# Performance work log

Measured on AMD Instinct MI355X. Metric: run time of the kernel, lower is better.

The kernel has to match this reference:

```python
import jax, jax.numpy as jnp
import numpy as np

H = 12          # num heads
D = 768         # embed dim
HD = D // H     # head dim
SCALE = HD ** -0.5
NEG = -(3.0 ** 39)  # matches torch's triu(1) * -3.0**39 mask value


def setup_inputs() -> dict:
    key = jax.random.key(0)
    ks = jax.random.split(key, 9)
    B, S = 4, 1024
    lim = 1.0 / np.sqrt(D)
    def lin(k):
        kw, kb = jax.random.split(k)
        W = jax.random.uniform(kw, (D, D), jnp.float32, -lim, lim)  # [out,in]
        b = jax.random.uniform(kb, (D,), jnp.float32, -lim, lim)
        return W, b
    Wq, bq = lin(ks[0]); Wk, bk = lin(ks[1]); Wv, bv = lin(ks[2]); Wo, bo = lin(ks[3])
    hidden_states = jax.random.normal(ks[4], (B, S, D), jnp.float32)
    return {"hidden_states": hidden_states,
            "Wq": Wq, "bq": bq, "Wk": Wk, "bk": bk,
            "Wv": Wv, "bv": bv, "Wo": Wo, "bo": bo}


def reference(hidden_states, Wq, bq, Wk, bk, Wv, bv, Wo, bo):
    B, S, _ = hidden_states.shape
    split = lambda x: x.reshape(B, S, H, HD).transpose(0, 2, 1, 3)  # [B,H,S,HD]
    q = split(hidden_states @ Wq.T + bq) * SCALE
    k = split(hidden_states @ Wk.T + bk)
    v = split(hidden_states @ Wv.T + bv)
    scores = jnp.einsum('bhqd,bhkd->bhqk', q, k)
    causal_mask = jnp.triu(jnp.full((S, S), NEG, hidden_states.dtype), k=1)
    scores = scores + causal_mask  # broadcast over [B,H]
    probs = jax.nn.softmax(scores, axis=-1)
    out = jnp.einsum('bhqk,bhkd->bhqd', probs, v)
    out = out.transpose(0, 2, 1, 3).reshape(B, S, H * HD)
    return out @ Wo.T + bo
```

## Files before the change

kernel.cpp:

```cpp
#include <hip/hip_runtime.h>

#define NH 12
#define DM 768
#define HD 64
#define BB 4
#define SS 1024
#define MTOT (BB*SS)
#define ATT_SCALE 0.125f
#define NEGMASK (-4.0525551530189755e18f)

typedef __attribute__((ext_vector_type(8))) short short8;
typedef __attribute__((ext_vector_type(4))) float floatx4;
typedef __attribute__((ext_vector_type(4))) unsigned short ushort4v;

__device__ __forceinline__ float bf2f(unsigned short u){
    union { unsigned int i; float f; } x; x.i = ((unsigned int)u) << 16; return x.f;
}
__device__ __forceinline__ unsigned short f2bf(float f){
    union { float f; unsigned int i; } x; x.f = f;
    unsigned int i = x.i;
    return (unsigned short)((i + 0x7FFFu + ((i >> 16) & 1u)) >> 16);
}

#define XQ4 (MTOT*DM/4)
#define WQ4 (DM*DM/4)

__global__ __launch_bounds__(256) void convert_bf16(
    const float* __restrict__ X,
    const float* __restrict__ Wq, const float* __restrict__ Wk,
    const float* __restrict__ Wv, const float* __restrict__ Wo,
    unsigned short* __restrict__ Xb,
    unsigned short* __restrict__ Wqb, unsigned short* __restrict__ Wkb,
    unsigned short* __restrict__ Wvb, unsigned short* __restrict__ Wob)
{
    const int idx = blockIdx.x * 256 + threadIdx.x;
    const float* s; unsigned short* d; int off;
    if (idx < XQ4) { s = X; d = Xb; off = idx; }
    else {
        const int r = idx - XQ4;
        const int wsel = r / WQ4;
        off = r - wsel * WQ4;
        s = (wsel==0)?Wq:(wsel==1)?Wk:(wsel==2)?Wv:Wo;
        d = (wsel==0)?Wqb:(wsel==1)?Wkb:(wsel==2)?Wvb:Wob;
    }
    const float4 v = ((const float4*)s)[off];
    ushort4v o;
    o[0] = f2bf(v.x); o[1] = f2bf(v.y); o[2] = f2bf(v.z); o[3] = f2bf(v.w);
    ((ushort4v*)d)[off] = o;
}

__global__ __launch_bounds__(256) void qkv_mfma(
    const unsigned short* __restrict__ Xb,
    const unsigned short* __restrict__ Wqb,
    const unsigned short* __restrict__ Wkb,
    const unsigned short* __restrict__ Wvb,
    const float* __restrict__ bq, const float* __restrict__ bk,
    const float* __restrict__ bv,
    unsigned short* __restrict__ qout,
    unsigned short* __restrict__ kout,
    unsigned short* __restrict__ vout)
{
    const int which = blockIdx.z;
    const int n0 = blockIdx.x * 64;
    const int m0 = blockIdx.y * 128;
    const unsigned short* W = (which==0) ? Wqb : (which==1) ? Wkb : Wvb;
    const float* bias = (which==0) ? bq : (which==1) ? bk : bv;
    const float scl = (which==0) ? ATT_SCALE : 1.0f;

    __shared__ unsigned short As[128*32];
    __shared__ unsigned short Bs[64*32];

    const int t = threadIdx.x;
    const int w = t >> 6, lane = t & 63;
    const int c = lane & 15, g = lane >> 4;
    const int wr = w >> 1, wc = w & 1;

    floatx4 acc[4][2] = {};

    const int srow = lane >> 2;
    const int ske  = (lane & 3) * 8;

    for (int k0 = 0; k0 < DM; k0 += 32) {
        __syncthreads();
        #pragma unroll
        for (int j = 0; j < 2; ++j) {
            const int row = w*32 + j*16 + srow;
            __builtin_amdgcn_global_load_lds(
                (const __attribute__((address_space(1))) unsigned int*)
                    (Xb + (size_t)(m0 + row) * DM + k0 + ske),
                (__attribute__((address_space(3))) unsigned int*)
                    (As + (w*32 + j*16) * 32),
                16, 0, 0);
        }
        {
            const int row = w*16 + srow;
            __builtin_amdgcn_global_load_lds(
                (const __attribute__((address_space(1))) unsigned int*)
                    (W + (size_t)(n0 + row) * DM + k0 + ske),
                (__attribute__((address_space(3))) unsigned int*)
                    (Bs + (w*16) * 32),
                16, 0, 0);
        }
        __syncthreads();

        short8 af[4], bfr[2];
        #pragma unroll
        for (int mi = 0; mi < 4; ++mi)
            af[mi] = *(const short8*)(As + (wr*64 + mi*16 + c)*32 + g*8);
        #pragma unroll
        for (int ni = 0; ni < 2; ++ni)
            bfr[ni] = *(const short8*)(Bs + (wc*32 + ni*16 + c)*32 + g*8);
        #pragma unroll
        for (int mi = 0; mi < 4; ++mi)
            #pragma unroll
            for (int ni = 0; ni < 2; ++ni)
                acc[mi][ni] = __builtin_amdgcn_mfma_f32_16x16x32_bf16(
                    af[mi], bfr[ni], acc[mi][ni], 0, 0, 0);
    }

    #pragma unroll
    for (int mi = 0; mi < 4; ++mi) {
        #pragma unroll
        for (int r = 0; r < 4; ++r) {
            const int m = m0 + wr*64 + mi*16 + g*4 + r;
            const int b = m >> 10, s = m & 1023;
            #pragma unroll
            for (int ni = 0; ni < 2; ++ni) {
                const int n = n0 + wc*32 + ni*16 + c;
                const int h = n >> 6, hd = n & 63;
                const float val = (acc[mi][ni][r] + bias[n]) * scl;
                if (which == 2)
                    vout[(((size_t)(b*NH + h))*HD + hd)*SS + s] = f2bf(val);
                else if (which == 1)
                    kout[(((size_t)(b*NH + h))*SS + s)*HD + hd] = f2bf(val);
                else
                    qout[(((size_t)(b*NH + h))*SS + s)*HD + hd] = f2bf(val);
            }
        }
    }
}

__device__ __forceinline__ void stage_tile(
    const unsigned short* __restrict__ Kp,
    const unsigned short* __restrict__ VTp,
    int k0, int w, int lane,
    unsigned short* __restrict__ Ks,
    unsigned short* __restrict__ Vs)
{
    const int rsub = lane >> 3;
    const int cc   = (lane & 7) ^ rsub;
    #pragma unroll
    for (int j = 0; j < 2; ++j) {
        const int r = w*16 + j*8 + rsub;
        __builtin_amdgcn_global_load_lds(
            (const __attribute__((address_space(1))) unsigned int*)
                (Kp + (size_t)(k0 + r) * HD + cc*8),
            (__attribute__((address_space(3))) unsigned int*)
                (Ks + (w*16 + j*8) * HD),
            16, 0, 0);
        __builtin_amdgcn_global_load_lds(
            (const __attribute__((address_space(1))) unsigned int*)
                (VTp + (size_t)r * SS + k0 + cc*8),
            (__attribute__((address_space(3))) unsigned int*)
                (Vs + (w*16 + j*8) * HD),
            16, 0, 0);
    }
}

__device__ __forceinline__ void attn_process_tile(
    const unsigned short* __restrict__ Ks,
    const unsigned short* __restrict__ Vs,
    const short8 (&qf)[2],
    int k0, bool islast, int qg, int c, int g,
    float& m_c, float& l_c, floatx4 (&Oacc)[4],
    unsigned short* __restrict__ Pl)
{
    floatx4 S[4] = {};
    #pragma unroll
    for (int nf = 0; nf < 4; ++nf) {
        const int row = nf*16 + c;
        #pragma unroll
        for (int st = 0; st < 2; ++st) {
            const short8 kf = *(const short8*)(Ks + row*HD + (((g + 4*st) ^ (c & 7)) * 8));
            S[nf] = __builtin_amdgcn_mfma_f32_16x16x32_bf16(kf, qf[st], S[nf], 0, 0, 0);
        }
    }

    if (islast) {
        #pragma unroll
        for (int nf = 0; nf < 4; ++nf) {
            #pragma unroll
            for (int r = 0; r < 4; ++r) {
                const int key = k0 + nf*16 + g*4 + r;
                if (key > qg) S[nf][r] += NEGMASK;
            }
        }
    }

    float mx = -INFINITY;
    #pragma unroll
    for (int nf = 0; nf < 4; ++nf)
        #pragma unroll
        for (int r = 0; r < 4; ++r) mx = fmaxf(mx, S[nf][r]);
    mx = fmaxf(mx, __shfl_xor(mx, 16, 64));
    mx = fmaxf(mx, __shfl_xor(mx, 32, 64));
    const float mnew = fmaxf(m_c, mx);
    const float alpha = __expf(m_c - mnew);
    float sum = 0.0f;
    #pragma unroll
    for (int nf = 0; nf < 4; ++nf)
        #pragma unroll
        for (int r = 0; r < 4; ++r) {
            const float p = __expf(S[nf][r] - mnew);
            S[nf][r] = p;
            sum += p;
        }
    sum += __shfl_xor(sum, 16, 64);
    sum += __shfl_xor(sum, 32, 64);
    l_c = l_c * alpha + sum;
    m_c = mnew;
    #pragma unroll
    for (int nf = 0; nf < 4; ++nf)
        #pragma unroll
        for (int r = 0; r < 4; ++r) Oacc[nf][r] *= alpha;

    #pragma unroll
    for (int nf = 0; nf < 4; ++nf)
        #pragma unroll
        for (int r = 0; r < 4; ++r)
            Pl[c * 72 + nf*16 + g*4 + r] = f2bf(S[nf][r]);

    #pragma unroll
    for (int st = 0; st < 2; ++st) {
        const short8 pf = *(const short8*)(Pl + c * 72 + g*8 + 32*st);
        #pragma unroll
        for (int nf = 0; nf < 4; ++nf) {
            const int row = nf*16 + c;
            const short8 vf = *(const short8*)(Vs + row*HD + (((g + 4*st) ^ (c & 7)) * 8));
            Oacc[nf] = __builtin_amdgcn_mfma_f32_16x16x32_bf16(vf, pf, Oacc[nf], 0, 0, 0);
        }
    }
}

__global__ __launch_bounds__(256) void attn_mfma(
    const unsigned short* __restrict__ Q,
    const unsigned short* __restrict__ K,
    const unsigned short* __restrict__ VT,
    unsigned short* __restrict__ O)
{
    const int idx = blockIdx.x;
    const int bh  = idx % 48;
    const int z   = 15 - (idx / 48);
    const int q0  = z * 64;

    const unsigned short* Qp  = Q  + (size_t)bh * SS * HD;
    const unsigned short* Kp  = K  + (size_t)bh * SS * HD;
    const unsigned short* VTp = VT + (size_t)bh * HD * SS;

    __shared__ unsigned short Ks[2][64*HD];
    __shared__ unsigned short Vs[2][64*HD];
    __shared__ unsigned short Pl[4][16*72];

    const int t    = threadIdx.x;
    const int w    = t >> 6;
    const int lane = t & 63;
    const int c    = lane & 15;
    const int g    = lane >> 4;
    const int qg   = q0 + w*16 + c;

    short8 qf[2];
    #pragma unroll
    for (int st = 0; st < 2; ++st)
        qf[st] = *(const short8*)(Qp + (size_t)qg * HD + g*8 + 32*st);

    floatx4 Oacc[4] = {};
    float m_c = -INFINITY, l_c = 0.0f;

    const int ntile = z + 1;

    stage_tile(Kp, VTp, 0, w, lane, Ks[0], Vs[0]);
    __syncthreads();

    for (int kt = 0; kt < ntile; ++kt) {
        const int cur = kt & 1;
        if (kt + 1 < ntile)
            stage_tile(Kp, VTp, (kt+1)*64, w, lane, Ks[cur^1], Vs[cur^1]);
        attn_process_tile(Ks[cur], Vs[cur], qf, kt*64, kt == ntile-1,
                          qg, c, g, m_c, l_c, Oacc, Pl[w]);
        if (kt + 1 < ntile)
            __syncthreads();
    }

    const int b = bh / NH, h = bh % NH;
    const float inv = 1.0f / l_c;
    unsigned short* op = O + ((size_t)(b*SS + qg))*DM + h*HD;
    #pragma unroll
    for (int nf = 0; nf < 4; ++nf) {
        ushort4v o4;
        #pragma unroll
        for (int r = 0; r < 4; ++r) o4[r] = f2bf(Oacc[nf][r] * inv);
        *(ushort4v*)(op + nf*16 + g*4) = o4;
    }
}

__global__ __launch_bounds__(256) void out_mfma(
    const unsigned short* __restrict__ A,
    const unsigned short* __restrict__ Wb,
    const float* __restrict__ bias,
    float* __restrict__ outf)
{
    const int n0 = blockIdx.x * 64;
    const int m0 = blockIdx.y * 128;

    __shared__ unsigned short As[128*32];
    __shared__ unsigned short Bs[64*32];

    const int t = threadIdx.x;
    const int w = t >> 6, lane = t & 63;
    const int c = lane & 15, g = lane >> 4;
    const int wr = w >> 1, wc = w & 1;

    floatx4 acc[4][2] = {};

    const int srow = lane >> 2;
    const int ske  = (lane & 3) * 8;

    for (int k0 = 0; k0 < DM; k0 += 32) {
        __syncthreads();
        #pragma unroll
        for (int j = 0; j < 2; ++j) {
            const int row = w*32 + j*16 + srow;
            __builtin_amdgcn_global_load_lds(
                (const __attribute__((address_space(1))) unsigned int*)
                    (A + (size_t)(m0 + row) * DM + k0 + ske),
                (__attribute__((address_space(3))) unsigned int*)
                    (As + (w*32 + j*16) * 32),
                16, 0, 0);
        }
        {
            const int row = w*16 + srow;
            __builtin_amdgcn_global_load_lds(
                (const __attribute__((address_space(1))) unsigned int*)
                    (Wb + (size_t)(n0 + row) * DM + k0 + ske),
                (__attribute__((address_space(3))) unsigned int*)
                    (Bs + (w*16) * 32),
                16, 0, 0);
        }
        __syncthreads();

        short8 af[4], bfr[2];
        #pragma unroll
        for (int mi = 0; mi < 4; ++mi)
            af[mi] = *(const short8*)(As + (wr*64 + mi*16 + c)*32 + g*8);
        #pragma unroll
        for (int ni = 0; ni < 2; ++ni)
            bfr[ni] = *(const short8*)(Bs + (wc*32 + ni*16 + c)*32 + g*8);
        #pragma unroll
        for (int mi = 0; mi < 4; ++mi)
            #pragma unroll
            for (int ni = 0; ni < 2; ++ni)
                acc[mi][ni] = __builtin_amdgcn_mfma_f32_16x16x32_bf16(
                    af[mi], bfr[ni], acc[mi][ni], 0, 0, 0);
    }

    #pragma unroll
    for (int mi = 0; mi < 4; ++mi) {
        #pragma unroll
        for (int r = 0; r < 4; ++r) {
            const int m = m0 + wr*64 + mi*16 + g*4 + r;
            #pragma unroll
            for (int ni = 0; ni < 2; ++ni) {
                const int n = n0 + wc*32 + ni*16 + c;
                outf[(size_t)m * DM + n] = acc[mi][ni][r] + bias[n];
            }
        }
    }
}

extern "C" void kernel_launch(void* const* d_in, const int* in_sizes, int n_in,
                              void* d_out, int out_size, void* d_ws, size_t ws_size,
                              hipStream_t stream) {
    const float* X  = (const float*)d_in[0];
    const float* Wq = (const float*)d_in[1];
    const float* bq = (const float*)d_in[2];
    const float* Wk = (const float*)d_in[3];
    const float* bk = (const float*)d_in[4];
    const float* Wv = (const float*)d_in[5];
    const float* bv = (const float*)d_in[6];
    const float* Wo = (const float*)d_in[7];
    const float* bo = (const float*)d_in[8];
    float* out = (float*)d_out;

    const size_t elems = (size_t)MTOT * DM;
    const size_t welems = (size_t)DM * DM;
    unsigned short* q    = (unsigned short*)d_ws;
    unsigned short* k    = q    + elems;
    unsigned short* vt   = k    + elems;
    unsigned short* attn = vt   + elems;
    unsigned short* xb   = attn + elems;
    unsigned short* wqb  = xb   + elems;
    unsigned short* wkb  = wqb  + welems;
    unsigned short* wvb  = wkb  + welems;
    unsigned short* wob  = wvb  + welems;

    convert_bf16<<<dim3((XQ4 + 4*WQ4) / 256), 256, 0, stream>>>(
        X, Wq, Wk, Wv, Wo, xb, wqb, wkb, wvb, wob);
    qkv_mfma<<<dim3(12, 32, 3), 256, 0, stream>>>(
        xb, wqb, wkb, wvb, bq, bk, bv, q, k, vt);
    attn_mfma<<<dim3(768), 256, 0, stream>>>(q, k, vt, attn);
    out_mfma<<<dim3(12, 32), 256, 0, stream>>>(attn, wob, bo, out);
}
```

Baseline: 161.2 us.

## Widen GEMM tiles to 128x128 and double-buffer LDS in projection kernels

The QKV and output projection GEMMs now use 128x128 output tiles, with 4x4 MFMA accumulators per wave instead of 4x2. Shared-memory A and B buffers are double-buffered so the next k-slice's global-to-LDS load is issued before computing the current one, leaving one barrier per step. The QKV kernel treats the three contiguous bf16 weight matrices as one 2304-row matrix in a flat 18x32 grid. This gives more reuse per loaded tile and overlaps loads with compute, at the cost of more registers and LDS and far fewer blocks for the output GEMM (192), which may underfill the GPU.

```diff
diff --git a/kernel.cpp b/kernel.cpp
--- a/kernel.cpp
+++ b/kernel.cpp
@@ -49,73 +49,91 @@
     ((ushort4v*)d)[off] = o;
 }
 
+__device__ __forceinline__ void gemm_stage(
+    const unsigned short* __restrict__ A,
+    const unsigned short* __restrict__ Bm,
+    int m0, int n0, int k0, int w, int lane,
+    unsigned short* __restrict__ As, unsigned short* __restrict__ Bs)
+{
+    const int srow = lane >> 2;
+    const int ske  = (lane & 3) * 8;
+    #pragma unroll
+    for (int j = 0; j < 2; ++j) {
+        const int row = w*32 + j*16 + srow;
+        __builtin_amdgcn_global_load_lds(
+            (const __attribute__((address_space(1))) unsigned int*)
+                (A + (size_t)(m0 + row) * DM + k0 + ske),
+            (__attribute__((address_space(3))) unsigned int*)
+                (As + (w*32 + j*16) * 32),
+            16, 0, 0);
+        __builtin_amdgcn_global_load_lds(
+            (const __attribute__((address_space(1))) unsigned int*)
+                (Bm + (size_t)(n0 + row) * DM + k0 + ske),
+            (__attribute__((address_space(3))) unsigned int*)
+                (Bs + (w*32 + j*16) * 32),
+            16, 0, 0);
+    }
+}
+
+__device__ __forceinline__ void gemm_compute(
+    const unsigned short* __restrict__ As,
+    const unsigned short* __restrict__ Bs,
+    int wr, int wc, int c, int g, floatx4 (&acc)[4][4])
+{
+    short8 af[4], bfr[4];
+    #pragma unroll
+    for (int mi = 0; mi < 4; ++mi)
+        af[mi] = *(const short8*)(As + (wr*64 + mi*16 + c)*32 + g*8);
+    #pragma unroll
+    for (int ni = 0; ni < 4; ++ni)
+        bfr[ni] = *(const short8*)(Bs + (wc*64 + ni*16 + c)*32 + g*8);
+    #pragma unroll
+    for (int mi = 0; mi < 4; ++mi)
+        #pragma unroll
+        for (int ni = 0; ni < 4; ++ni)
+            acc[mi][ni] = __builtin_amdgcn_mfma_f32_16x16x32_bf16(
+                af[mi], bfr[ni], acc[mi][ni], 0, 0, 0);
+}
+
 __global__ __launch_bounds__(256) void qkv_mfma(
     const unsigned short* __restrict__ Xb,
-    const unsigned short* __restrict__ Wqb,
-    const unsigned short* __restrict__ Wkb,
-    const unsigned short* __restrict__ Wvb,
+    const unsigned short* __restrict__ Wqkv,
     const float* __restrict__ bq, const float* __restrict__ bk,
     const float* __restrict__ bv,
     unsigned short* __restrict__ qout,
     unsigned short* __restrict__ kout,
     unsigned short* __restrict__ vout)
 {
-    const int which = blockIdx.z;
-    const int n0 = blockIdx.x * 64;
+    const int bx = blockIdx.x;
+    const int which = bx / 6;
+    const int np0 = (bx % 6) * 128;
+    const int n0 = bx * 128;
     const int m0 = blockIdx.y * 128;
-    const unsigned short* W = (which==0) ? Wqb : (which==1) ? Wkb : Wvb;
+
     const float* bias = (which==0) ? bq : (which==1) ? bk : bv;
     const float scl = (which==0) ? ATT_SCALE : 1.0f;
 
-    __shared__ unsigned short As[128*32];
-    __shared__ unsigned short Bs[64*32];
+    __shared__ unsigned short As[2][128*32];
+    __shared__ unsigned short Bs[2][128*32];
 
     const int t = threadIdx.x;
     const int w = t >> 6, lane = t & 63;
     const int c = lane & 15, g = lane >> 4;
     const int wr = w >> 1, wc = w & 1;
 
-    floatx4 acc[4][2] = {};
-
-    const int srow = lane >> 2;
-    const int ske  = (lane & 3) * 8;
-
-    for (int k0 = 0; k0 < DM; k0 += 32) {
-        __syncthreads();
-        #pragma unroll
-        for (int j = 0; j < 2; ++j) {
-            const int row = w*32 + j*16 + srow;
-            __builtin_amdgcn_global_load_lds(
-                (const __attribute__((address_space(1))) unsigned int*)
-                    (Xb + (size_t)(m0 + row) * DM + k0 + ske),
-                (__attribute__((address_space(3))) unsigned int*)
-                    (As + (w*32 + j*16) * 32),
-                16, 0, 0);
-        }
-        {
-            const int row = w*16 + srow;
-            __builtin_amdgcn_global_load_lds(
-                (const __attribute__((address_space(1))) unsigned int*)
-                    (W + (size_t)(n0 + row) * DM + k0 + ske),
-                (__attribute__((address_space(3))) unsigned int*)
-                    (Bs + (w*16) * 32),
-                16, 0, 0);
-        }
-        __syncthreads();
-
-        short8 af[4], bfr[2];
-        #pragma unroll
-        for (int mi = 0; mi < 4; ++mi)
-            af[mi] = *(const short8*)(As + (wr*64 + mi*16 + c)*32 + g*8);
-        #pragma unroll
-        for (int ni = 0; ni < 2; ++ni)
-            bfr[ni] = *(const short8*)(Bs + (wc*32 + ni*16 + c)*32 + g*8);
-        #pragma unroll
-        for (int mi = 0; mi < 4; ++mi)
-            #pragma unroll
-            for (int ni = 0; ni < 2; ++ni)
-                acc[mi][ni] = __builtin_amdgcn_mfma_f32_16x16x32_bf16(
-                    af[mi], bfr[ni], acc[mi][ni], 0, 0, 0);
+    floatx4 acc[4][4] = {};
+
+    gemm_stage(Xb, Wqkv, m0, n0, 0, w, lane, As[0], Bs[0]);
+    __syncthreads();
+
+    #pragma unroll 2
+    for (int kt = 0; kt < 24; ++kt) {
+        const int cur = kt & 1;
+        if (kt + 1 < 24)
+            gemm_stage(Xb, Wqkv, m0, n0, (kt+1)*32, w, lane, As[cur^1], Bs[cur^1]);
+        gemm_compute(As[cur], Bs[cur], wr, wc, c, g, acc);
+        if (kt + 1 < 24)
+            __syncthreads();
     }
 
     #pragma unroll
@@ -125,10 +143,10 @@
             const int m = m0 + wr*64 + mi*16 + g*4 + r;
             const int b = m >> 10, s = m & 1023;
             #pragma unroll
-            for (int ni = 0; ni < 2; ++ni) {
-                const int n = n0 + wc*32 + ni*16 + c;
-                const int h = n >> 6, hd = n & 63;
-                const float val = (acc[mi][ni][r] + bias[n]) * scl;
+            for (int ni = 0; ni < 4; ++ni) {
+                const int np = np0 + wc*64 + ni*16 + c;
+                const int h = np >> 6, hd = np & 63;
+                const float val = (acc[mi][ni][r] + bias[np]) * scl;
                 if (which == 2)
                     vout[(((size_t)(b*NH + h))*HD + hd)*SS + s] = f2bf(val);
                 else if (which == 1)
@@ -309,58 +327,30 @@
     const float* __restrict__ bias,
     float* __restrict__ outf)
 {
-    const int n0 = blockIdx.x * 64;
+    const int n0 = blockIdx.x * 128;
     const int m0 = blockIdx.y * 128;
 
-    __shared__ unsigned short As[128*32];
-    __shared__ unsigned short Bs[64*32];
+    __shared__ unsigned short As[2][128*32];
+    __shared__ unsigned short Bs[2][128*32];
 
     const int t = threadIdx.x;
     const int w = t >> 6, lane = t & 63;
     const int c = lane & 15, g = lane >> 4;
     const int wr = w >> 1, wc = w & 1;
 
-    floatx4 acc[4][2] = {};
-
-    const int srow = lane >> 2;
-    const int ske  = (lane & 3) * 8;
-
-    for (int k0 = 0; k0 < DM; k0 += 32) {
-        __syncthreads();
-        #pragma unroll
-        for (int j = 0; j < 2; ++j) {
-            const int row = w*32 + j*16 + srow;
-            __builtin_amdgcn_global_load_lds(
-                (const __attribute__((address_space(1))) unsigned int*)
-                    (A + (size_t)(m0 + row) * DM + k0 + ske),
-                (__attribute__((address_space(3))) unsigned int*)
-                    (As + (w*32 + j*16) * 32),
-                16, 0, 0);
-        }
-        {
-            const int row = w*16 + srow;
-            __builtin_amdgcn_global_load_lds(
-                (const __attribute__((address_space(1))) unsigned int*)
-                    (Wb + (size_t)(n0 + row) * DM + k0 + ske),
-                (__attribute__((address_space(3))) unsigned int*)
-                    (Bs + (w*16) * 32),
-                16, 0, 0);
-        }
-        __syncthreads();
-
-        short8 af[4], bfr[2];
-        #pragma unroll
-        for (int mi = 0; mi < 4; ++mi)
-            af[mi] = *(const short8*)(As + (wr*64 + mi*16 + c)*32 + g*8);
-        #pragma unroll
-        for (int ni = 0; ni < 2; ++ni)
-            bfr[ni] = *(const short8*)(Bs + (wc*32 + ni*16 + c)*32 + g*8);
-        #pragma unroll
-        for (int mi = 0; mi < 4; ++mi)
-            #pragma unroll
-            for (int ni = 0; ni < 2; ++ni)
-                acc[mi][ni] = __builtin_amdgcn_mfma_f32_16x16x32_bf16(
-                    af[mi], bfr[ni], acc[mi][ni], 0, 0, 0);
+    floatx4 acc[4][4] = {};
+
+    gemm_stage(A, Wb, m0, n0, 0, w, lane, As[0], Bs[0]);
+    __syncthreads();
+
+    #pragma unroll 2
+    for (int kt = 0; kt < 24; ++kt) {
+        const int cur = kt & 1;
+        if (kt + 1 < 24)
+            gemm_stage(A, Wb, m0, n0, (kt+1)*32, w, lane, As[cur^1], Bs[cur^1]);
+        gemm_compute(As[cur], Bs[cur], wr, wc, c, g, acc);
+        if (kt + 1 < 24)
+            __syncthreads();
     }
 
     #pragma unroll
@@ -369,8 +359,8 @@
         for (int r = 0; r < 4; ++r) {
             const int m = m0 + wr*64 + mi*16 + g*4 + r;
             #pragma unroll
-            for (int ni = 0; ni < 2; ++ni) {
-                const int n = n0 + wc*32 + ni*16 + c;
+            for (int ni = 0; ni < 4; ++ni) {
+                const int n = n0 + wc*64 + ni*16 + c;
                 outf[(size_t)m * DM + n] = acc[mi][ni][r] + bias[n];
             }
         }
@@ -405,8 +395,8 @@
 
     convert_bf16<<<dim3((XQ4 + 4*WQ4) / 256), 256, 0, stream>>>(
         X, Wq, Wk, Wv, Wo, xb, wqb, wkb, wvb, wob);
-    qkv_mfma<<<dim3(12, 32, 3), 256, 0, stream>>>(
-        xb, wqb, wkb, wvb, bq, bk, bv, q, k, vt);
+    qkv_mfma<<<dim3(18, 32), 256, 0, stream>>>(
+        xb, wqb, bq, bk, bv, q, k, vt);
     attn_mfma<<<dim3(768), 256, 0, stream>>>(q, k, vt, attn);
-    out_mfma<<<dim3(12, 32), 256, 0, stream>>>(attn, wob, bo, out);
-}
+    out_mfma<<<dim3(6, 32), 256, 0, stream>>>(attn, wob, bo, out);
+}
```

Result: slower. 177.1 us (+9.8%).
